# Optimization experiments

Measured on AMD Instinct MI355X. Metric: run time of the kernel, lower is better.

The kernel has to match this reference:

```python
import jax, jax.numpy as jnp
import numpy as np

K = 20          # knn neighbors (args.k)
BN_EPS = 1e-5   # torch BatchNorm default
LN_EPS = 1e-6


def _bn(x, g, b, axes):
    # training-mode batchnorm over `axes`, channel dim = 1
    m = x.mean(axes, keepdims=True)
    v = x.var(axes, keepdims=True)
    shp = [1] * x.ndim
    shp[1] = x.shape[1]
    return g.reshape(shp) * (x - m) * jax.lax.rsqrt(v + BN_EPS) + b.reshape(shp)


def _lrelu(x):
    return jnp.where(x >= 0, x, 0.2 * x)


def _graph_feature(x, k):
    # x: [B,C,N] -> [B,2C,N,k]  (knn gather + (neighbor-center, center) concat)
    B, C, N = x.shape
    inner = -2.0 * jnp.einsum('bcn,bcm->bnm', x, x)
    xx = jnp.sum(x * x, axis=1)                       # [B,N]
    pd = -xx[:, :, None] - inner - xx[:, None, :]     # negative sq. distance
    idx = jax.lax.top_k(pd, k)[1]                     # [B,N,k]
    xt = jnp.transpose(x, (0, 2, 1))                  # [B,N,C]
    feat = xt[jnp.arange(B)[:, None, None], idx]      # [B,N,k,C] gather
    ctr = xt[:, :, None, :]
    out = jnp.concatenate([feat - ctr, jnp.broadcast_to(ctr, feat.shape)], axis=-1)
    return jnp.transpose(out, (0, 3, 1, 2))


def _conv2d_block(x, w, g, b):
    # 1x1 conv2d (no bias) + BN2d + LeakyReLU(0.2)
    y = jnp.einsum('bcnk,oc->bonk', x, w)
    return _lrelu(_bn(y, g, b, (0, 2, 3)))


def _conv1d_block(x, w, g, b):
    y = jnp.einsum('bcl,oc->bol', x, w)
    return _lrelu(_bn(y, g, b, (0, 2)))


def _squash(t):
    sn = jnp.sum(t * t, axis=-1, keepdims=True)
    return sn * t / ((1.0 + sn) * jnp.sqrt(sn))


def _forward(data, l, dw1, dg1, db1, dw2, dg2, db2, dw3, dg3, db3,
             lin_w, ln_w, ln_b, caps_W,
             cw1, cg1, cb1, cw2, cg2, cb2, cw3, cw4, cg4, cb4, cw5, cg5, cb5):
    B, _, N = data.shape
    # ---- DGCNN encoder ----
    x = _conv2d_block(_graph_feature(data, K), dw1, dg1, db1)
    x1 = x.max(axis=-1)                               # [B,64,N]
    x = _conv2d_block(_graph_feature(x1, K), dw2, dg2, db2)
    x2 = x.max(axis=-1)                               # [B,64,N]
    x = _conv2d_block(_graph_feature(x2, K), dw3, dg3, db3)
    x3 = x.max(axis=-1)                               # [B,128,N]
    feat = jnp.transpose(jnp.concatenate([x1, x2, x3], axis=1), (0, 2, 1))  # [B,N,256]
    h = jnp.einsum('bnc,oc->bno', feat, lin_w)        # [B,N,40]
    mu = h.mean(axis=(1, 2), keepdims=True)
    var = h.var(axis=(1, 2), keepdims=True)
    encoder = jax.nn.relu(ln_w * (h - mu) * jax.lax.rsqrt(var + LN_EPS) + ln_b)  # [B,1024,40]
    # ---- Latent capsule layer (3-iter dynamic routing) ----
    u_hat = jnp.einsum('lpvd,bpd->blpv', caps_W, encoder)  # [B,40,1024,64]
    u_det = jax.lax.stop_gradient(u_hat)
    b_ij = jnp.zeros((B, caps_W.shape[0], caps_W.shape[1]), encoder.dtype)
    v = None
    for it in range(3):
        c = jax.nn.softmax(b_ij, axis=1)
        if it == 2:
            v = _squash(jnp.einsum('blp,blpv->blv', c, u_hat))
        else:
            v = _squash(jnp.einsum('blp,blpv->blv', c, u_det))
            b_ij = b_ij + jnp.einsum('blv,blpv->blp', v, u_det)
    latent = v                                        # [B,40,64]
    # ---- segmentation head ----
    emb = jnp.einsum('bpd,bdv->bpv', encoder, latent) # [B,1024,64]
    emb = emb.max(axis=-1, keepdims=True)             # [B,1024,1]
    lab = _conv1d_block(l.reshape(B, -1, 1), cw1, cg1, cb1)  # [B,64,1]
    emb = jnp.concatenate([emb, lab], axis=1)         # [B,1088,1]
    emb = jnp.tile(emb, (1, 1, N))                    # [B,1088,N]
    emb = jnp.concatenate([emb, jnp.transpose(encoder, (0, 2, 1))], axis=1)  # [B,1128,N]
    r = _conv1d_block(emb, cw2, cg2, cb2)
    r = _conv1d_block(r, cw3, cg2, cb2)               # conv3 shares bn2 params
    r = _conv1d_block(r, cw4, cg4, cb4)
    r = _conv1d_block(r, cw5, cg5, cb5)
    return r                                          # [B,50,N]


def setup_inputs() -> dict:
    key = jax.random.key(0)
    ks = jax.random.split(key, 16)
    B, N = 32, 1024
    f = jnp.float32
    rn = lambda k, s: 0.05 * jax.random.normal(k, s, dtype=f)
    return dict(
        data=jax.random.normal(ks[0], (B, 3, N), dtype=f),
        l=jax.random.uniform(ks[1], (B, 16), dtype=f),
        dw1=rn(ks[2], (64, 6)), dg1=jnp.ones(64, f), db1=jnp.zeros(64, f),
        dw2=rn(ks[3], (64, 128)), dg2=jnp.ones(64, f), db2=jnp.zeros(64, f),
        dw3=rn(ks[4], (128, 128)), dg3=jnp.ones(128, f), db3=jnp.zeros(128, f),
        lin_w=rn(ks[5], (40, 256)),
        ln_w=jnp.ones((N, 40), f), ln_b=jnp.zeros((N, 40), f),
        caps_W=0.01 * jax.random.normal(ks[6], (40, 1024, 64, 40), dtype=f),
        cw1=rn(ks[7], (64, 16)), cg1=jnp.ones(64, f), cb1=jnp.zeros(64, f),
        cw2=rn(ks[8], (256, 1128)), cg2=jnp.ones(256, f), cb2=jnp.zeros(256, f),
        cw3=rn(ks[9], (256, 256)),
        cw4=rn(ks[10], (128, 256)), cg4=jnp.ones(128, f), cb4=jnp.zeros(128, f),
        cw5=rn(ks[11], (50, 128)), cg5=jnp.ones(50, f), cb5=jnp.zeros(50, f),
    )


def reference(data, l, dw1, dg1, db1, dw2, dg2, db2, dw3, dg3, db3,
              lin_w, ln_w, ln_b, caps_W,
              cw1, cg1, cb1, cw2, cg2, cb2, cw3, cw4, cg4, cb4, cw5, cg5, cb5):
    return _forward(data, l, dw1, dg1, db1, dw2, dg2, db2, dw3, dg3, db3,
                    lin_w, ln_w, ln_b, caps_W,
                    cw1, cg1, cb1, cw2, cg2, cb2, cw3, cw4, cg4, cb4, cw5, cg5, cb5)
```

## Files before the change

### kernel.cpp

```cpp
#include <hip/hip_runtime.h>
#include <math.h>

constexpr int NB = 32, NN = 1024, KNN = 20;
constexpr int RTOT = NB * NN;

constexpr size_t SZ_BIG = (size_t)NB * NN * 40 * 64;
constexpr size_t O_BIG  = 0;
constexpr size_t O_XT0  = O_BIG + SZ_BIG;
constexpr size_t O_XT1  = O_XT0 + (size_t)RTOT * 4;
constexpr size_t O_XT2  = O_XT1 + (size_t)RTOT * 64;
constexpr size_t O_XT3  = O_XT2 + (size_t)RTOT * 64;
constexpr size_t O_XX   = O_XT3 + (size_t)RTOT * 128;
constexpr size_t O_IDX  = O_XX + RTOT;
constexpr size_t O_WC1  = O_IDX + (size_t)RTOT * KNN;
constexpr size_t O_WC2  = O_WC1 + 512;
constexpr size_t O_WC3  = O_WC2 + 8192;
constexpr size_t O_LWT  = O_WC3 + 16384;
constexpr size_t O_C2T  = O_LWT + 16384;
constexpr size_t O_C3T  = O_C2T + 10240;
constexpr size_t O_C4T  = O_C3T + 65536;
constexpr size_t O_C5T  = O_C4T + 32768;
constexpr size_t O_H    = O_C5T + 8192;
constexpr size_t O_LNST = O_H + (size_t)RTOT * 64;
constexpr size_t O_BSUM = O_LNST + 64;
constexpr size_t O_BSQ  = O_BSUM + 256;
constexpr size_t O_SCL  = O_BSQ + 256;
constexpr size_t O_SHF  = O_SCL + 256;
constexpr size_t O_SACC = O_SHF + 256;
constexpr size_t O_VB   = O_SACC + 81920;
constexpr size_t O_BIJ  = O_VB + 81920;
constexpr size_t O_EMB  = O_BIJ + (size_t)NB * 40 * NN;
constexpr size_t O_LAB  = O_EMB + RTOT;
constexpr size_t O_BASE = O_LAB + 2048;
constexpr size_t O_PS   = O_BIJ;
constexpr size_t O_PQ   = O_BIJ + 262144;
constexpr size_t O_PB   = O_XT1;
constexpr size_t O_PBU  = O_XT1;

__device__ __forceinline__ float lrelu(float z) { return fmaxf(z, 0.2f * z); }

__device__ __forceinline__ float key2f(unsigned u)
{
    unsigned b = (u & 0x80000000u) ? (u ^ 0x80000000u) : ~u;
    return __uint_as_float(b);
}

__global__ void k_wt(const float* __restrict__ src, float* __restrict__ dst,
                     int K, int On, int SS, int coff, int DS, int ooff, int Oreal)
{
    int i = blockIdx.x * 256 + threadIdx.x;
    if (i >= K * On) return;
    int c = i / On, o = i - c * On;
    dst[(size_t)c * DS + ooff + o] = (o < Oreal) ? src[(size_t)o * SS + coff + c] : 0.f;
}

__global__ void k_data_t(const float* __restrict__ d, float* __restrict__ xt)
{
    int i = blockIdx.x * 256 + threadIdx.x;
    if (i >= RTOT) return;
    int b = i >> 10, n = i & 1023;
#pragma unroll
    for (int c = 0; c < 3; ++c) xt[(size_t)i * 4 + c] = d[((size_t)b * 3 + c) * NN + n];
    xt[(size_t)i * 4 + 3] = 0.f;
}

template<int C, int CS>
__global__ void k_rownorm(const float* __restrict__ X, float* __restrict__ xx)
{
    int i = blockIdx.x * 256 + threadIdx.x;
    if (i >= RTOT) return;
    const float* p = X + (size_t)i * CS;
    float s = 0.f;
#pragma unroll
    for (int c = 0; c < C; ++c) s = fmaf(p[c], p[c], s);
    xx[i] = s;
}

template<int CS>
__global__ __launch_bounds__(256) void k_dist(const float* __restrict__ X,
    const float* __restrict__ xx, float* __restrict__ D)
{
    __shared__ float As[16][68];
    __shared__ float Bs[16][68];
    int b = blockIdx.z;
    int r0 = blockIdx.x * 64, m0 = blockIdx.y * 64;
    const float* Xb = X + (size_t)b * NN * CS;
    int t = threadIdx.x;
    int tx = t & 15, ty = t >> 4;
    float acc[4][4] = {};
    for (int k0 = 0; k0 < CS; k0 += 16) {
        __syncthreads();
        {
            int row = t >> 2, kb = (t & 3) * 4;
#pragma unroll
            for (int u = 0; u < 4; ++u) {
                int k = k0 + kb + u;
                As[kb + u][row] = (k < CS) ? Xb[(size_t)(r0 + row) * CS + k] : 0.f;
                Bs[kb + u][row] = (k < CS) ? Xb[(size_t)(m0 + row) * CS + k] : 0.f;
            }
        }
        __syncthreads();
#pragma unroll
        for (int k = 0; k < 16; ++k) {
            float4 a = *(const float4*)&As[k][ty * 4];
            float4 bb = *(const float4*)&Bs[k][tx * 4];
            float av[4] = {a.x, a.y, a.z, a.w};
            float bv[4] = {bb.x, bb.y, bb.z, bb.w};
#pragma unroll
            for (int i = 0; i < 4; ++i)
#pragma unroll
                for (int j = 0; j < 4; ++j)
                    acc[i][j] = fmaf(av[i], bv[j], acc[i][j]);
        }
    }
    const float* xxb = xx + b * NN + m0 + tx * 4;
    float x0 = xxb[0], x1 = xxb[1], x2 = xxb[2], x3 = xxb[3];
#pragma unroll
    for (int i = 0; i < 4; ++i) {
        float4 o4 = make_float4(2.f * acc[i][0] - x0, 2.f * acc[i][1] - x1,
                                2.f * acc[i][2] - x2, 2.f * acc[i][3] - x3);
        *(float4*)&D[((size_t)b * NN + r0 + ty * 4 + i) * NN + m0 + tx * 4] = o4;
    }
}

__global__ __launch_bounds__(256) void k_sel(const float* __restrict__ D,
                                             int* __restrict__ idxb)
{
    int gw = blockIdx.x * 4 + (threadIdx.x >> 6);
    int lane = threadIdx.x & 63;
    const float* drow = D + (size_t)gw * NN;
    float vr[16];
#pragma unroll
    for (int j = 0; j < 16; ++j) vr[j] = drow[j * 64 + lane];

    unsigned lo = 0x007FFFFFu;
    unsigned hi = 0xFF800000u;
#pragma unroll 1
    while (hi - lo > 1u) {
        unsigned mid = lo + ((hi - lo) >> 1);
        float tm = key2f(mid);
        int c = 0;
#pragma unroll
        for (int j = 0; j < 16; ++j) c += __popcll(__ballot(vr[j] > tm));
        if (c < KNN) hi = mid; else lo = mid;
    }
    float t = key2f(hi);

    int* outp = idxb + (size_t)gw * KNN;
    unsigned long long mylow = (1ull << lane) - 1ull;
    int base = 0;
#pragma unroll
    for (int j = 0; j < 16; ++j) {
        unsigned long long bmask = __ballot(vr[j] > t);
        if (vr[j] > t) outp[base + __popcll(bmask & mylow)] = j * 64 + lane;
        base += __popcll(bmask);
    }
#pragma unroll 1
    for (int j = 0; j < 16 && base < KNN; ++j) {
        unsigned long long bmask = __ballot(vr[j] == t);
        int pre = __popcll(bmask & mylow);
        if (vr[j] == t && base + pre < KNN) outp[base + pre] = j * 64 + lane;
        base += __popcll(bmask);
    }
}

template<bool ACT, bool BIAS>
__global__ __launch_bounds__(256) void k_gemm(const float* __restrict__ X,
    const float* __restrict__ W, float* __restrict__ Y, int K, int OC, int XS,
    const float* __restrict__ scale, const float* __restrict__ shift,
    const float* __restrict__ bias)
{
    __shared__ float Xs[16][68];
    __shared__ float Ws[16][64];
    int r0 = blockIdx.x * 64, o0 = blockIdx.y * 64;
    int t = threadIdx.x;
    int tx = t & 15, ty = t >> 4;
    float acc[4][4] = {};
    for (int k0 = 0; k0 < K; k0 += 16) {
        __syncthreads();
        {
            int row = t >> 2, kb = (t & 3) * 4;
#pragma unroll
            for (int u = 0; u < 4; ++u) {
                int k = k0 + kb + u;
                float v = 0.f;
                if (k < K) {
                    v = X[(size_t)(r0 + row) * XS + k];
                    if (ACT) { float z = fmaf(v, scale[k], shift[k]); v = fmaxf(z, 0.2f * z); }
                }
                Xs[kb + u][row] = v;
            }
            int kw = t >> 4, ow = (t & 15) * 4;
            float4 wv = make_float4(0.f, 0.f, 0.f, 0.f);
            if (k0 + kw < K) wv = *(const float4*)&W[(size_t)(k0 + kw) * OC + o0 + ow];
            *(float4*)&Ws[kw][ow] = wv;
        }
        __syncthreads();
#pragma unroll
        for (int k = 0; k < 16; ++k) {
            float4 a = *(const float4*)&Xs[k][ty * 4];
            float4 bb = *(const float4*)&Ws[k][tx * 4];
            float av[4] = {a.x, a.y, a.z, a.w};
            float bvv[4] = {bb.x, bb.y, bb.z, bb.w};
#pragma unroll
            for (int i = 0; i < 4; ++i)
#pragma unroll
                for (int j = 0; j < 4; ++j)
                    acc[i][j] = fmaf(av[i], bvv[j], acc[i][j]);
        }
    }
#pragma unroll
    for (int i = 0; i < 4; ++i) {
        int r = r0 + ty * 4 + i;
        float4 o4;
        float* po = (float*)&o4;
#pragma unroll
        for (int j = 0; j < 4; ++j) {
            float v = acc[i][j];
            if (BIAS) v += bias[(size_t)(r >> 10) * OC + o0 + tx * 4 + j];
            po[j] = v;
        }
        *(float4*)&Y[(size_t)r * OC + o0 + tx * 4] = o4;
    }
}

template<int O>
__global__ __launch_bounds__(256) void k_gather(const float* __restrict__ Z,
    const int* __restrict__ idxb, float* __restrict__ xo,
    float* __restrict__ part_s, float* __restrict__ part_q)
{
    constexpr int OL = O / 64;
    __shared__ float rs[4][O], rq[4][O];
    int b = blockIdx.y, nt = blockIdx.x;
    int t = threadIdx.x, lane = t & 63, w = t >> 6;
    float ps[OL] = {}, pq[OL] = {};
    for (int i = 0; i < 4; ++i) {
        int n = nt * 16 + w * 4 + i;
        size_t r = (size_t)b * NN + n;
        float zd[OL], ym[OL];
#pragma unroll
        for (int j = 0; j < OL; ++j) {
            int o = lane + j * 64;
            zd[j] = Z[r * (2 * O) + O + o] - Z[r * (2 * O) + o];
            ym[j] = -3.4e38f;
        }
        int midx[KNN];
        {
            const int4* ip = (const int4*)&idxb[r * KNN];
#pragma unroll
            for (int q = 0; q < 5; ++q) {
                int4 t4 = ip[q];
                midx[4 * q + 0] = t4.x; midx[4 * q + 1] = t4.y;
                midx[4 * q + 2] = t4.z; midx[4 * q + 3] = t4.w;
            }
        }
#pragma unroll
        for (int k = 0; k < KNN; ++k) {
            size_t rm = (size_t)b * NN + midx[k];
#pragma unroll
            for (int j = 0; j < OL; ++j) {
                float y = Z[rm * (2 * O) + lane + j * 64] + zd[j];
                ym[j] = fmaxf(ym[j], y);
                ps[j] += y; pq[j] = fmaf(y, y, pq[j]);
            }
        }
#pragma unroll
        for (int j = 0; j < OL; ++j) xo[r * O + lane + j * 64] = ym[j];
    }
#pragma unroll
    for (int j = 0; j < OL; ++j) { rs[w][lane + j * 64] = ps[j]; rq[w][lane + j * 64] = pq[j]; }
    __syncthreads();
    if (w == 0) {
        int blk = blockIdx.y * 64 + blockIdx.x;
#pragma unroll
        for (int j = 0; j < OL; ++j) {
            int o = lane + j * 64;
            part_s[(size_t)o * 2048 + blk] = rs[0][o] + rs[1][o] + rs[2][o] + rs[3][o];
            part_q[(size_t)o * 2048 + blk] = rq[0][o] + rq[1][o] + rq[2][o] + rq[3][o];
        }
    }
}

__global__ void k_bnfin2(const float* __restrict__ part_s, const float* __restrict__ part_q,
                         const float* __restrict__ g, const float* __restrict__ bb,
                         float* __restrict__ scale, float* __restrict__ shift,
                         int OC, float invM, float eps)
{
    int o = blockIdx.x * blockDim.x + threadIdx.x;
    if (o >= OC) return;
    const float* ps = part_s + (size_t)o * 2048;
    const float* pq = part_q + (size_t)o * 2048;
    float s0 = 0.f, s1 = 0.f, s2 = 0.f, s3 = 0.f;
    float q0 = 0.f, q1 = 0.f, q2 = 0.f, q3 = 0.f;
    for (int i = 0; i < 2048; i += 4) {
        s0 += ps[i]; s1 += ps[i + 1]; s2 += ps[i + 2]; s3 += ps[i + 3];
        q0 += pq[i]; q1 += pq[i + 1]; q2 += pq[i + 2]; q3 += pq[i + 3];
    }
    float s = (s0 + s1) + (s2 + s3);
    float q = (q0 + q1) + (q2 + q3);
    float mu = s * invM;
    float var = q * invM - mu * mu;
    float sc = g[o] * rsqrtf(var + eps);
    scale[o] = sc; shift[o] = bb[o] - mu * sc;
}

__global__ void k_bnfin(const float* __restrict__ sums, const float* __restrict__ sumsq,
                        const float* __restrict__ g, const float* __restrict__ bb,
                        float* __restrict__ scale, float* __restrict__ shift,
                        int OC, float invM, float eps)
{
    int o = blockIdx.x * blockDim.x + threadIdx.x;
    if (o >= OC) return;
    float mu = sums[o] * invM;
    float var = sumsq[o] * invM - mu * mu;
    float sc = g[o] * rsqrtf(var + eps);
    scale[o] = sc; shift[o] = bb[o] - mu * sc;
}

__global__ void k_bnapply(float* __restrict__ x, const float* __restrict__ scale,
                          const float* __restrict__ shift, int total, int O)
{
    int i = blockIdx.x * 256 + threadIdx.x;
    if (i >= total) return;
    int o = i & (O - 1);
    x[i] = lrelu(fmaf(x[i], scale[o], shift[o]));
}

__global__ void k_concat(const float* __restrict__ x1, const float* __restrict__ x2,
                         const float* __restrict__ x3, float* __restrict__ f)
{
    int i = blockIdx.x * 256 + threadIdx.x;
    if (i >= RTOT * 256) return;
    int r = i >> 8, c = i & 255;
    float v;
    if (c < 64) v = x1[(size_t)r * 64 + c];
    else if (c < 128) v = x2[(size_t)r * 64 + c - 64];
    else v = x3[(size_t)r * 128 + c - 128];
    f[(size_t)i] = v;
}

__global__ __launch_bounds__(256) void k_lnstats(const float* __restrict__ h, float* __restrict__ st)
{
    __shared__ float rsm[256], rqm[256];
    int b = blockIdx.x, t = threadIdx.x;
    float s = 0.f, q = 0.f;
    for (int i = t; i < 40960; i += 256) {
        int n = i / 40, o = i - n * 40;
        float v = h[((size_t)b * NN + n) * 64 + o];
        s += v; q = fmaf(v, v, q);
    }
    rsm[t] = s; rqm[t] = q; __syncthreads();
    for (int off = 128; off; off >>= 1) {
        if (t < off) { rsm[t] += rsm[t + off]; rqm[t] += rqm[t + off]; }
        __syncthreads();
    }
    if (t == 0) {
        float mu = rsm[0] / 40960.f;
        float var = rqm[0] / 40960.f - mu * mu;
        st[2 * b] = mu; st[2 * b + 1] = rsqrtf(var + 1e-6f);
    }
}

__global__ void k_lnapply(float* __restrict__ h, const float* __restrict__ lnw,
                          const float* __restrict__ lnb, const float* __restrict__ st)
{
    int i = blockIdx.x * 256 + threadIdx.x;
    if (i >= NB * NN * 40) return;
    int b = i / 40960, rem = i - b * 40960, n = rem / 40, o = rem - n * 40;
    float mu = st[2 * b], rstd = st[2 * b + 1];
    size_t a = ((size_t)b * NN + n) * 64 + o;
    float v = fmaf((h[a] - mu) * rstd, lnw[n * 40 + o], lnb[n * 40 + o]);
    h[a] = fmaxf(v, 0.f);
}

__global__ __launch_bounds__(64) void k_uhat(const float* __restrict__ enc,
    const float* __restrict__ caps, float* __restrict__ U, float* __restrict__ pbu)
{
    __shared__ float clt[40 * 68];
    int pc = blockIdx.x, l = blockIdx.y;
    int lane = threadIdx.x;
    int vg = lane & 7, bg = lane >> 3;
    int v0 = vg * 8, b0 = bg * 4;
    float spart[4][8] = {};
#pragma unroll 1
    for (int pi = 0; pi < 16; ++pi) {
        int p = pc * 16 + pi;
        const float4* cp4 = (const float4*)(caps + ((size_t)l * NN + p) * 2560);
#pragma unroll
        for (int k = 0; k < 10; ++k) {
            int i4 = lane + k * 64;
            float4 cv = cp4[i4];
            int e0 = i4 * 4;
            int v = e0 / 40;
            int d0 = e0 - v * 40;
            clt[(d0 + 0) * 68 + v] = cv.x;
            clt[(d0 + 1) * 68 + v] = cv.y;
            clt[(d0 + 2) * 68 + v] = cv.z;
            clt[(d0 + 3) * 68 + v] = cv.w;
        }
        float acc[4][8] = {};
#pragma unroll
        for (int d4 = 0; d4 < 10; ++d4) {
            float4 e4[4];
#pragma unroll
            for (int i = 0; i < 4; ++i)
                e4[i] = *(const float4*)&enc[((size_t)(b0 + i) * NN + p) * 64 + d4 * 4];
#pragma unroll
            for (int dd = 0; dd < 4; ++dd) {
                int d = d4 * 4 + dd;
                float4 c0 = *(const float4*)&clt[d * 68 + v0];
                float4 c1 = *(const float4*)&clt[d * 68 + v0 + 4];
                float cv[8] = {c0.x, c0.y, c0.z, c0.w, c1.x, c1.y, c1.z, c1.w};
#pragma unroll
                for (int i = 0; i < 4; ++i) {
                    float e = ((const float*)&e4[i])[dd];
#pragma unroll
                    for (int j = 0; j < 8; ++j)
                        acc[i][j] = fmaf(e, cv[j], acc[i][j]);
                }
            }
        }
#pragma unroll
        for (int i = 0; i < 4; ++i) {
            float* up = &U[((size_t)(b0 + i) * NN + p) * 2560 + l * 64 + v0];
            float4 o0 = make_float4(acc[i][0], acc[i][1], acc[i][2], acc[i][3]);
            float4 o1 = make_float4(acc[i][4], acc[i][5], acc[i][6], acc[i][7]);
            *(float4*)up = o0;
            *(float4*)(up + 4) = o1;
#pragma unroll
            for (int j = 0; j < 8; ++j) spart[i][j] += acc[i][j];
        }
    }
    float* pb = pbu + (size_t)pc * 81920;
#pragma unroll
    for (int i = 0; i < 4; ++i) {
        float4 s0 = make_float4(spart[i][0], spart[i][1], spart[i][2], spart[i][3]);
        float4 s1 = make_float4(spart[i][4], spart[i][5], spart[i][6], spart[i][7]);
        float* dst = &pb[(size_t)(b0 + i) * 2560 + l * 64 + v0];
        *(float4*)dst = s0;
        *(float4*)(dst + 4) = s1;
    }
}

template<int MODE>
__global__ __launch_bounds__(256, 4) void k_route(const float* __restrict__ U,
    const float* __restrict__ vprev, const float* __restrict__ bin,
    float* __restrict__ bout, float* __restrict__ pbuf)
{
    __shared__ float vl[2560];
    __shared__ float red[4][1280];
    int b = blockIdx.x, pc = blockIdx.y;
    int t = threadIdx.x, lane = t & 63, w = t >> 6;
    for (int i = t; i < 2560; i += 256) vl[i] = vprev[(size_t)b * 2560 + i];
    __syncthreads();
    float4 acc[10];
#pragma unroll
    for (int it = 0; it < 10; ++it) acc[it] = make_float4(0.f, 0.f, 0.f, 0.f);
    int lgrp = lane >> 4;
#pragma unroll 1
    for (int pi = 0; pi < 8; ++pi) {
        int p = pc * 32 + w * 8 + pi;
        const float4* up4 = (const float4*)(U + ((size_t)b * NN + p) * 2560);
        float4 u[10];
#pragma unroll
        for (int it = 0; it < 10; ++it) u[it] = up4[it * 64 + lane];
        float pd[10];
#pragma unroll
        for (int it = 0; it < 10; ++it) {
            float4 vv = *(const float4*)&vl[it * 256 + lane * 4];
            float s = u[it].x * vv.x;
            s = fmaf(u[it].y, vv.y, s);
            s = fmaf(u[it].z, vv.z, s);
            s = fmaf(u[it].w, vv.w, s);
            s += __shfl_xor(s, 1, 64);
            s += __shfl_xor(s, 2, 64);
            s += __shfl_xor(s, 4, 64);
            s += __shfl_xor(s, 8, 64);
            pd[it] = s;
        }
        if (MODE == 1) {
            if ((lane & 15) == 0) {
#pragma unroll
                for (int it = 0; it < 10; ++it)
                    bout[((size_t)b * 40 + it * 4 + lgrp) * NN + p] = pd[it];
            }
        } else {
#pragma unroll
            for (int it = 0; it < 10; ++it)
                pd[it] += bin[((size_t)b * 40 + it * 4 + lgrp) * NN + p];
        }
        float mx = -3.4e38f;
#pragma unroll
        for (int it = 0; it < 10; ++it) {
            float m = pd[it];
            m = fmaxf(m, __shfl_xor(m, 16, 64));
            m = fmaxf(m, __shfl_xor(m, 32, 64));
            mx = fmaxf(mx, m);
        }
        float eo[10]; float se = 0.f;
#pragma unroll
        for (int it = 0; it < 10; ++it) {
            float e = expf(pd[it] - mx);
            eo[it] = e;
            float sg = e;
            sg += __shfl_xor(sg, 16, 64);
            sg += __shfl_xor(sg, 32, 64);
            se += sg;
        }
        float inv = 1.f / se;
#pragma unroll
        for (int it = 0; it < 10; ++it) {
            float wgt = eo[it] * inv;
            acc[it].x = fmaf(wgt, u[it].x, acc[it].x);
            acc[it].y = fmaf(wgt, u[it].y, acc[it].y);
            acc[it].z = fmaf(wgt, u[it].z, acc[it].z);
            acc[it].w = fmaf(wgt, u[it].w, acc[it].w);
        }
    }
    float* pb = pbuf + ((size_t)pc * NB + b) * 2560;
#pragma unroll 1
    for (int h = 0; h < 2; ++h) {
        __syncthreads();
#pragma unroll
        for (int it = 0; it < 5; ++it)
            *(float4*)&red[w][it * 256 + lane * 4] = acc[h * 5 + it];
        __syncthreads();
        if (w == 0) {
#pragma unroll
            for (int it = 0; it < 5; ++it) {
                int idx = it * 256 + lane * 4;
                float4 a0 = *(const float4*)&red[0][idx];
                float4 a1 = *(const float4*)&red[1][idx];
                float4 a2 = *(const float4*)&red[2][idx];
                float4 a3 = *(const float4*)&red[3][idx];
                float4 o = make_float4((a0.x + a1.x) + (a2.x + a3.x),
                                       (a0.y + a1.y) + (a2.y + a3.y),
                                       (a0.z + a1.z) + (a2.z + a3.z),
                                       (a0.w + a1.w) + (a2.w + a3.w));
                *(float4*)&pb[h * 1280 + idx] = o;
            }
        }
    }
}

template<int NCH>
__global__ void k_sredN(const float* __restrict__ pbuf, float* __restrict__ sac)
{
    int i4 = blockIdx.x * 256 + threadIdx.x;
    if (i4 >= NB * 640) return;
    const float4* pb4 = (const float4*)pbuf;
    float4 s = make_float4(0.f, 0.f, 0.f, 0.f);
#pragma unroll 4
    for (int pc = 0; pc < NCH; ++pc) {
        float4 v = pb4[(size_t)pc * (NB * 640) + i4];
        s.x += v.x; s.y += v.y; s.z += v.z; s.w += v.w;
    }
    ((float4*)sac)[i4] = s;
}

__global__ void k_squash(const float* __restrict__ s_in, float* __restrict__ vout, float premul)
{
    int i = blockIdx.x * 256 + threadIdx.x;
    if (i >= NB * 40) return;
    const float* sp = s_in + (size_t)i * 64;
    float* vp = vout + (size_t)i * 64;
    float sn = 0.f;
    for (int v = 0; v < 64; ++v) { float tv = sp[v] * premul; sn = fmaf(tv, tv, sn); }
    float f = sn / ((1.f + sn) * sqrtf(sn));
    for (int v = 0; v < 64; ++v) vp[v] = sp[v] * premul * f;
}

__global__ __launch_bounds__(256) void k_emb(const float* __restrict__ enc,
    const float* __restrict__ lat, float* __restrict__ embm)
{
    __shared__ float latl[2560];
    int b = blockIdx.x, pt = blockIdx.y;
    int t = threadIdx.x, lane = t & 63, w = t >> 6;
    for (int i = t; i < 2560; i += 256) latl[i] = lat[(size_t)b * 2560 + i];
    __syncthreads();
    for (int i = 0; i < 32; ++i) {
        int p = pt * 128 + w * 32 + i;
        const float* ep = enc + ((size_t)b * NN + p) * 64;
        float acc = 0.f;
#pragma unroll
        for (int d = 0; d < 40; ++d) acc = fmaf(ep[d], latl[d * 64 + lane], acc);
        float mx = acc;
#pragma unroll
        for (int s = 32; s; s >>= 1) mx = fmaxf(mx, __shfl_xor(mx, s, 64));
        if (lane == 0) embm[(size_t)b * NN + p] = mx;
    }
}

__global__ __launch_bounds__(64) void k_lab(const float* __restrict__ lin,
    const float* __restrict__ w, const float* __restrict__ g, const float* __restrict__ bb,
    float* __restrict__ lab)
{
    int o = threadIdx.x;
    float ys[32]; float s = 0.f, q = 0.f;
#pragma unroll
    for (int b = 0; b < 32; ++b) {
        float y = 0.f;
#pragma unroll
        for (int c = 0; c < 16; ++c) y = fmaf(lin[b * 16 + c], w[o * 16 + c], y);
        ys[b] = y; s += y; q = fmaf(y, y, q);
    }
    float mu = s / 32.f, var = q / 32.f - mu * mu;
    float sc = g[o] * rsqrtf(var + 1e-5f);
    float sh = bb[o] - mu * sc;
#pragma unroll
    for (int b = 0; b < 32; ++b) lab[b * 64 + o] = lrelu(fmaf(ys[b], sc, sh));
}

__global__ __launch_bounds__(256) void k_base2(const float* __restrict__ em,
    const float* __restrict__ lab, const float* __restrict__ cw2, float* __restrict__ base)
{
    __shared__ float eml[1024];
    __shared__ float lbl[64];
    int b = blockIdx.x, t = threadIdx.x;
    for (int i = t; i < 1024; i += 256) eml[i] = em[(size_t)b * NN + i];
    if (t < 64) lbl[t] = lab[b * 64 + t];
    __syncthreads();
    const float* wr = cw2 + (size_t)t * 1128;
    float acc = 0.f;
    for (int c = 0; c < 1024; ++c) acc = fmaf(wr[c], eml[c], acc);
#pragma unroll
    for (int c = 0; c < 64; ++c) acc = fmaf(wr[1024 + c], lbl[c], acc);
    base[b * 256 + t] = acc;
}

__global__ __launch_bounds__(256) void k_colstats(const float* __restrict__ Y,
    float* __restrict__ sums, float* __restrict__ sumsq, int OC)
{
    __shared__ float rs[4][64], rq[4][64];
    int chunk = blockIdx.x, o0 = blockIdx.y * 64;
    int t = threadIdx.x, lane = t & 63, w = t >> 6;
    int o = o0 + lane;
    float s = 0.f, q = 0.f;
    for (int j = 0; j < 64; ++j) {
        int r = chunk * 256 + w * 64 + j;
        float v = Y[(size_t)r * OC + o];
        s += v; q = fmaf(v, v, q);
    }
    rs[w][lane] = s; rq[w][lane] = q;
    __syncthreads();
    if (w == 0) {
        atomicAdd(&sums[o], rs[0][lane] + rs[1][lane] + rs[2][lane] + rs[3][lane]);
        atomicAdd(&sumsq[o], rq[0][lane] + rq[1][lane] + rq[2][lane] + rq[3][lane]);
    }
}

__global__ void k_out(const float* __restrict__ Y, const float* __restrict__ scale,
                      const float* __restrict__ shift, float* __restrict__ out)
{
    int i = blockIdx.x * 256 + threadIdx.x;
    if (i >= NB * 50 * NN) return;
    int n = i & 1023, rest = i >> 10;
    int o = rest % 50, b = rest / 50;
    float y = Y[((size_t)b * NN + n) * 64 + o];
    out[i] = lrelu(fmaf(y, scale[o], shift[o]));
}

extern "C" void kernel_launch(void* const* d_in, const int* in_sizes, int n_in,
                              void* d_out, int out_size, void* d_ws, size_t ws_size,
                              hipStream_t stream)
{
    const float* data = (const float*)d_in[0];
    const float* lin  = (const float*)d_in[1];
    const float* dw1  = (const float*)d_in[2];
    const float* dg1  = (const float*)d_in[3];
    const float* db1  = (const float*)d_in[4];
    const float* dw2  = (const float*)d_in[5];
    const float* dg2  = (const float*)d_in[6];
    const float* db2  = (const float*)d_in[7];
    const float* dw3  = (const float*)d_in[8];
    const float* dg3  = (const float*)d_in[9];
    const float* db3  = (const float*)d_in[10];
    const float* lw   = (const float*)d_in[11];
    const float* lnw  = (const float*)d_in[12];
    const float* lnb  = (const float*)d_in[13];
    const float* caps = (const float*)d_in[14];
    const float* cw1  = (const float*)d_in[15];
    const float* cg1  = (const float*)d_in[16];
    const float* cb1  = (const float*)d_in[17];
    const float* cw2  = (const float*)d_in[18];
    const float* cg2  = (const float*)d_in[19];
    const float* cb2  = (const float*)d_in[20];
    const float* cw3  = (const float*)d_in[21];
    const float* cw4  = (const float*)d_in[22];
    const float* cg4  = (const float*)d_in[23];
    const float* cb4  = (const float*)d_in[24];
    const float* cw5  = (const float*)d_in[25];
    const float* cg5  = (const float*)d_in[26];
    const float* cb5  = (const float*)d_in[27];
    float* out = (float*)d_out;
    float* ws = (float*)d_ws;

    float* big  = ws + O_BIG;
    float* xt0  = ws + O_XT0;
    float* xt1  = ws + O_XT1;
    float* xt2  = ws + O_XT2;
    float* xt3  = ws + O_XT3;
    float* xxp  = ws + O_XX;
    int*   idxb = (int*)(ws + O_IDX);
    float* wc1  = ws + O_WC1;
    float* wc2  = ws + O_WC2;
    float* wc3  = ws + O_WC3;
    float* lwt  = ws + O_LWT;
    float* c2t  = ws + O_C2T;
    float* c3t  = ws + O_C3T;
    float* c4t  = ws + O_C4T;
    float* c5t  = ws + O_C5T;
    float* hbuf = ws + O_H;
    float* lnst = ws + O_LNST;
    float* bsum = ws + O_BSUM;
    float* bsq  = ws + O_BSQ;
    float* scl  = ws + O_SCL;
    float* shf  = ws + O_SHF;
    float* sac  = ws + O_SACC;
    float* vb   = ws + O_VB;
    float* bij  = ws + O_BIJ;
    float* embm = ws + O_EMB;
    float* labp = ws + O_LAB;
    float* basep= ws + O_BASE;
    float* psP  = ws + O_PS;
    float* pqP  = ws + O_PQ;
    float* pbuf = ws + O_PB;
    float* pbu  = ws + O_PBU;
    float* Dbuf = big;
    float* Z    = big;
    float* U    = big;
    float* yb1  = big;
    float* yb2  = big + 8388608;

    k_wt<<<1,   256, 0, stream>>>(dw1, wc1, 3, 64, 6, 0, 128, 0, 64);
    k_wt<<<1,   256, 0, stream>>>(dw1, wc1, 3, 64, 6, 3, 128, 64, 64);
    k_wt<<<16,  256, 0, stream>>>(dw2, wc2, 64, 64, 128, 0, 128, 0, 64);
    k_wt<<<16,  256, 0, stream>>>(dw2, wc2, 64, 64, 128, 64, 128, 64, 64);
    k_wt<<<32,  256, 0, stream>>>(dw3, wc3, 64, 128, 128, 0, 256, 0, 128);
    k_wt<<<32,  256, 0, stream>>>(dw3, wc3, 64, 128, 128, 64, 256, 128, 128);
    k_wt<<<64,  256, 0, stream>>>(lw,  lwt, 256, 64, 256, 0, 64, 0, 40);
    k_wt<<<40,  256, 0, stream>>>(cw2, c2t, 40, 256, 1128, 1088, 256, 0, 256);
    k_wt<<<256, 256, 0, stream>>>(cw3, c3t, 256, 256, 256, 0, 256, 0, 256);
    k_wt<<<128, 256, 0, stream>>>(cw4, c4t, 256, 128, 256, 0, 128, 0, 128);
    k_wt<<<32,  256, 0, stream>>>(cw5, c5t, 128, 64, 128, 0, 64, 0, 50);
    k_data_t<<<128, 256, 0, stream>>>(data, xt0);

    k_rownorm<3, 4><<<128, 256, 0, stream>>>(xt0, xxp);
    k_dist<4><<<dim3(16, 16, 32), 256, 0, stream>>>(xt0, xxp, Dbuf);
    k_sel<<<8192, 256, 0, stream>>>(Dbuf, idxb);
    k_gemm<false, false><<<dim3(512, 2), 256, 0, stream>>>(xt0, wc1, Z, 3, 128, 4, nullptr, nullptr, nullptr);
    k_gather<64><<<dim3(64, 32), 256, 0, stream>>>(Z, idxb, xt1, psP, pqP);
    k_bnfin2<<<1, 64, 0, stream>>>(psP, pqP, dg1, db1, scl, shf, 64, 1.f / 655360.f, 1e-5f);
    k_bnapply<<<8192, 256, 0, stream>>>(xt1, scl, shf, RTOT * 64, 64);

    k_rownorm<64, 64><<<128, 256, 0, stream>>>(xt1, xxp);
    k_dist<64><<<dim3(16, 16, 32), 256, 0, stream>>>(xt1, xxp, Dbuf);
    k_sel<<<8192, 256, 0, stream>>>(Dbuf, idxb);
    k_gemm<false, false><<<dim3(512, 2), 256, 0, stream>>>(xt1, wc2, Z, 64, 128, 64, nullptr, nullptr, nullptr);
    k_gather<64><<<dim3(64, 32), 256, 0, stream>>>(Z, idxb, xt2, psP, pqP);
    k_bnfin2<<<1, 64, 0, stream>>>(psP, pqP, dg2, db2, scl, shf, 64, 1.f / 655360.f, 1e-5f);
    k_bnapply<<<8192, 256, 0, stream>>>(xt2, scl, shf, RTOT * 64, 64);

    k_rownorm<64, 64><<<128, 256, 0, stream>>>(xt2, xxp);
    k_dist<64><<<dim3(16, 16, 32), 256, 0, stream>>>(xt2, xxp, Dbuf);
    k_sel<<<8192, 256, 0, stream>>>(Dbuf, idxb);
    k_gemm<false, false><<<dim3(512, 4), 256, 0, stream>>>(xt2, wc3, Z, 64, 256, 64, nullptr, nullptr, nullptr);
    k_gather<128><<<dim3(64, 32), 256, 0, stream>>>(Z, idxb, xt3, psP, pqP);
    k_bnfin2<<<1, 128, 0, stream>>>(psP, pqP, dg3, db3, scl, shf, 128, 1.f / 655360.f, 1e-5f);
    k_bnapply<<<16384, 256, 0, stream>>>(xt3, scl, shf, RTOT * 128, 128);

    k_concat<<<32768, 256, 0, stream>>>(xt1, xt2, xt3, big);
    k_gemm<false, false><<<dim3(512, 1), 256, 0, stream>>>(big, lwt, hbuf, 256, 64, 256, nullptr, nullptr, nullptr);
    k_lnstats<<<32, 256, 0, stream>>>(hbuf, lnst);
    k_lnapply<<<5120, 256, 0, stream>>>(hbuf, lnw, lnb, lnst);

    k_uhat<<<dim3(64, 40), 64, 0, stream>>>(hbuf, caps, U, pbu);
    k_sredN<64><<<80, 256, 0, stream>>>(pbu, sac);
    k_squash<<<5, 256, 0, stream>>>(sac, vb, 1.f / 40.f);
    k_route<1><<<dim3(32, 32), 256, 0, stream>>>(U, vb, nullptr, bij, pbuf);
    k_sredN<32><<<80, 256, 0, stream>>>(pbuf, sac);
    k_squash<<<5, 256, 0, stream>>>(sac, vb, 1.f);
    k_route<2><<<dim3(32, 32), 256, 0, stream>>>(U, vb, bij, nullptr, pbuf);
    k_sredN<32><<<80, 256, 0, stream>>>(pbuf, sac);
    k_squash<<<5, 256, 0, stream>>>(sac, vb, 1.f);

    k_emb<<<dim3(32, 8), 256, 0, stream>>>(hbuf, vb, embm);
    k_lab<<<1, 64, 0, stream>>>(lin, cw1, cg1, cb1, labp);
    k_base2<<<32, 256, 0, stream>>>(embm, labp, cw2, basep);

    k_gemm<false, true><<<dim3(512, 4), 256, 0, stream>>>(hbuf, c2t, yb1, 40, 256, 64, nullptr, nullptr, basep);
    hipMemsetAsync(bsum, 0, 512 * 4, stream);
    k_colstats<<<dim3(128, 4), 256, 0, stream>>>(yb1, bsum, bsq, 256);
    k_bnfin<<<1, 256, 0, stream>>>(bsum, bsq, cg2, cb2, scl, shf, 256, 1.f / 32768.f, 1e-5f);

    k_gemm<true, false><<<dim3(512, 4), 256, 0, stream>>>(yb1, c3t, yb2, 256, 256, 256, scl, shf, nullptr);
    hipMemsetAsync(bsum, 0, 512 * 4, stream);
    k_colstats<<<dim3(128, 4), 256, 0, stream>>>(yb2, bsum, bsq, 256);
    k_bnfin<<<1, 256, 0, stream>>>(bsum, bsq, cg2, cb2, scl, shf, 256, 1.f / 32768.f, 1e-5f);

    k_gemm<true, false><<<dim3(512, 2), 256, 0, stream>>>(yb2, c4t, yb1, 256, 128, 256, scl, shf, nullptr);
    hipMemsetAsync(bsum, 0, 512 * 4, stream);
    k_colstats<<<dim3(128, 2), 256, 0, stream>>>(yb1, bsum, bsq, 128);
    k_bnfin<<<1, 256, 0, stream>>>(bsum, bsq, cg4, cb4, scl, shf, 128, 1.f / 32768.f, 1e-5f);

    k_gemm<true, false><<<dim3(512, 1), 256, 0, stream>>>(yb1, c5t, yb2, 128, 64, 128, scl, shf, nullptr);
    hipMemsetAsync(bsum, 0, 512 * 4, stream);
    k_colstats<<<dim3(128, 1), 256, 0, stream>>>(yb2, bsum, bsq, 64);
    k_bnfin<<<1, 256, 0, stream>>>(bsum, bsq, cg5, cb5, scl, shf, 50, 1.f / 32768.f, 1e-5f);

    k_out<<<6400, 256, 0, stream>>>(yb2, scl, shf, out);
}
```

Measured before the change: 1.755 ms.

## Fuse small kernels to cut launch count and drop atomics/memsets in BN stats

Merges the eleven weight-transpose launches into one kernel and folds the row-norm computation into the data transpose and BN-apply kernels. Squash is fused into the capsule partial-sum reduction, and the label MLP is merged into k_base2. Column statistics now write per-chunk partials that bnfin3 reduces, which removes the atomics and memsets. The aim is to cut launch overhead and extra passes over memory, at the cost of k_base2 recomputing the label BN in every block.

Result: faster. 1.708 ms (-2.6%).

```diff
diff --git a/kernel.cpp b/kernel.cpp
--- a/kernel.cpp
+++ b/kernel.cpp
@@ -45,34 +45,50 @@
     return __uint_as_float(b);
 }
 
-__global__ void k_wt(const float* __restrict__ src, float* __restrict__ dst,
-                     int K, int On, int SS, int coff, int DS, int ooff, int Oreal)
-{
-    int i = blockIdx.x * 256 + threadIdx.x;
+__device__ __forceinline__ void wt_do(const float* __restrict__ src, float* __restrict__ dst,
+                                      int i, int K, int On, int SS, int coff, int DS, int ooff, int Oreal)
+{
     if (i >= K * On) return;
     int c = i / On, o = i - c * On;
     dst[(size_t)c * DS + ooff + o] = (o < Oreal) ? src[(size_t)o * SS + coff + c] : 0.f;
 }
 
-__global__ void k_data_t(const float* __restrict__ d, float* __restrict__ xt)
+__global__ __launch_bounds__(256) void k_wtall(
+    const float* __restrict__ dw1, const float* __restrict__ dw2, const float* __restrict__ dw3,
+    const float* __restrict__ lw,  const float* __restrict__ cw2, const float* __restrict__ cw3,
+    const float* __restrict__ cw4, const float* __restrict__ cw5,
+    float* __restrict__ wc1, float* __restrict__ wc2, float* __restrict__ wc3,
+    float* __restrict__ lwt, float* __restrict__ c2t, float* __restrict__ c3t,
+    float* __restrict__ c4t, float* __restrict__ c5t)
+{
+    int bid = blockIdx.x, t = threadIdx.x;
+    if      (bid < 1)   wt_do(dw1, wc1, (bid - 0) * 256 + t,   3, 64, 6, 0, 128, 0, 64);
+    else if (bid < 2)   wt_do(dw1, wc1, (bid - 1) * 256 + t,   3, 64, 6, 3, 128, 64, 64);
+    else if (bid < 18)  wt_do(dw2, wc2, (bid - 2) * 256 + t,   64, 64, 128, 0, 128, 0, 64);
+    else if (bid < 34)  wt_do(dw2, wc2, (bid - 18) * 256 + t,  64, 64, 128, 64, 128, 64, 64);
+    else if (bid < 66)  wt_do(dw3, wc3, (bid - 34) * 256 + t,  64, 128, 128, 0, 256, 0, 128);
+    else if (bid < 98)  wt_do(dw3, wc3, (bid - 66) * 256 + t,  64, 128, 128, 64, 256, 128, 128);
+    else if (bid < 162) wt_do(lw,  lwt, (bid - 98) * 256 + t,  256, 64, 256, 0, 64, 0, 40);
+    else if (bid < 202) wt_do(cw2, c2t, (bid - 162) * 256 + t, 40, 256, 1128, 1088, 256, 0, 256);
+    else if (bid < 458) wt_do(cw3, c3t, (bid - 202) * 256 + t, 256, 256, 256, 0, 256, 0, 256);
+    else if (bid < 586) wt_do(cw4, c4t, (bid - 458) * 256 + t, 256, 128, 256, 0, 128, 0, 128);
+    else                wt_do(cw5, c5t, (bid - 586) * 256 + t, 128, 64, 128, 0, 64, 0, 50);
+}
+
+__global__ void k_data_t(const float* __restrict__ d, float* __restrict__ xt,
+                         float* __restrict__ xx)
 {
     int i = blockIdx.x * 256 + threadIdx.x;
     if (i >= RTOT) return;
     int b = i >> 10, n = i & 1023;
-#pragma unroll
-    for (int c = 0; c < 3; ++c) xt[(size_t)i * 4 + c] = d[((size_t)b * 3 + c) * NN + n];
+    float s = 0.f;
+#pragma unroll
+    for (int c = 0; c < 3; ++c) {
+        float v = d[((size_t)b * 3 + c) * NN + n];
+        xt[(size_t)i * 4 + c] = v;
+        s = fmaf(v, v, s);
+    }
     xt[(size_t)i * 4 + 3] = 0.f;
-}
-
-template<int C, int CS>
-__global__ void k_rownorm(const float* __restrict__ X, float* __restrict__ xx)
-{
-    int i = blockIdx.x * 256 + threadIdx.x;
-    if (i >= RTOT) return;
-    const float* p = X + (size_t)i * CS;
-    float s = 0.f;
-#pragma unroll
-    for (int c = 0; c < C; ++c) s = fmaf(p[c], p[c], s);
     xx[i] = s;
 }
 
@@ -304,15 +320,25 @@
     scale[o] = sc; shift[o] = bb[o] - mu * sc;
 }
 
-__global__ void k_bnfin(const float* __restrict__ sums, const float* __restrict__ sumsq,
-                        const float* __restrict__ g, const float* __restrict__ bb,
-                        float* __restrict__ scale, float* __restrict__ shift,
-                        int OC, float invM, float eps)
+__global__ void k_bnfin3(const float* __restrict__ part_s, const float* __restrict__ part_q,
+                         const float* __restrict__ g, const float* __restrict__ bb,
+                         float* __restrict__ scale, float* __restrict__ shift,
+                         int OC, float invM, float eps)
 {
     int o = blockIdx.x * blockDim.x + threadIdx.x;
     if (o >= OC) return;
-    float mu = sums[o] * invM;
-    float var = sumsq[o] * invM - mu * mu;
+    const float* ps = part_s + (size_t)o * 128;
+    const float* pq = part_q + (size_t)o * 128;
+    float s0 = 0.f, s1 = 0.f, s2 = 0.f, s3 = 0.f;
+    float q0 = 0.f, q1 = 0.f, q2 = 0.f, q3 = 0.f;
+    for (int i = 0; i < 128; i += 4) {
+        s0 += ps[i]; s1 += ps[i + 1]; s2 += ps[i + 2]; s3 += ps[i + 3];
+        q0 += pq[i]; q1 += pq[i + 1]; q2 += pq[i + 2]; q3 += pq[i + 3];
+    }
+    float s = (s0 + s1) + (s2 + s3);
+    float q = (q0 + q1) + (q2 + q3);
+    float mu = s * invM;
+    float var = q * invM - mu * mu;
     float sc = g[o] * rsqrtf(var + eps);
     scale[o] = sc; shift[o] = bb[o] - mu * sc;
 }
@@ -324,6 +350,32 @@
     if (i >= total) return;
     int o = i & (O - 1);
     x[i] = lrelu(fmaf(x[i], scale[o], shift[o]));
+}
+
+__global__ __launch_bounds__(256) void k_bnapply_rn(float* __restrict__ x,
+    const float* __restrict__ scale, const float* __restrict__ shift,
+    float* __restrict__ xx)
+{
+    __shared__ float red[16][17];
+    int t = threadIdx.x;
+    int i4 = blockIdx.x * 256 + t;
+    int q = t & 15, lrow = t >> 4;
+    float4 v = ((float4*)x)[i4];
+    int o = q * 4;
+    v.x = lrelu(fmaf(v.x, scale[o + 0], shift[o + 0]));
+    v.y = lrelu(fmaf(v.y, scale[o + 1], shift[o + 1]));
+    v.z = lrelu(fmaf(v.z, scale[o + 2], shift[o + 2]));
+    v.w = lrelu(fmaf(v.w, scale[o + 3], shift[o + 3]));
+    ((float4*)x)[i4] = v;
+    float part = fmaf(v.w, v.w, fmaf(v.z, v.z, fmaf(v.y, v.y, v.x * v.x)));
+    red[lrow][q] = part;
+    __syncthreads();
+    if (t < 16) {
+        float s = 0.f;
+#pragma unroll
+        for (int j = 0; j < 16; ++j) s += red[t][j];
+        xx[blockIdx.x * 16 + t] = s;
+    }
 }
 
 __global__ void k_concat(const float* __restrict__ x1, const float* __restrict__ x2,
@@ -544,10 +596,14 @@
 }
 
 template<int NCH>
-__global__ void k_sredN(const float* __restrict__ pbuf, float* __restrict__ sac)
-{
-    int i4 = blockIdx.x * 256 + threadIdx.x;
-    if (i4 >= NB * 640) return;
+__global__ __launch_bounds__(256) void k_sredsq(const float* __restrict__ pbuf,
+    float* __restrict__ vout, float premul)
+{
+    __shared__ float red[16][17];
+    __shared__ float fac[16];
+    int t = threadIdx.x;
+    int i4 = blockIdx.x * 256 + t;
+    int q = t & 15, lrow = t >> 4;
     const float4* pb4 = (const float4*)pbuf;
     float4 s = make_float4(0.f, 0.f, 0.f, 0.f);
 #pragma unroll 4
@@ -555,19 +611,19 @@
         float4 v = pb4[(size_t)pc * (NB * 640) + i4];
         s.x += v.x; s.y += v.y; s.z += v.z; s.w += v.w;
     }
-    ((float4*)sac)[i4] = s;
-}
-
-__global__ void k_squash(const float* __restrict__ s_in, float* __restrict__ vout, float premul)
-{
-    int i = blockIdx.x * 256 + threadIdx.x;
-    if (i >= NB * 40) return;
-    const float* sp = s_in + (size_t)i * 64;
-    float* vp = vout + (size_t)i * 64;
-    float sn = 0.f;
-    for (int v = 0; v < 64; ++v) { float tv = sp[v] * premul; sn = fmaf(tv, tv, sn); }
-    float f = sn / ((1.f + sn) * sqrtf(sn));
-    for (int v = 0; v < 64; ++v) vp[v] = sp[v] * premul * f;
+    s.x *= premul; s.y *= premul; s.z *= premul; s.w *= premul;
+    float part = fmaf(s.w, s.w, fmaf(s.z, s.z, fmaf(s.y, s.y, s.x * s.x)));
+    red[lrow][q] = part;
+    __syncthreads();
+    if (t < 16) {
+        float sn = 0.f;
+#pragma unroll
+        for (int j = 0; j < 16; ++j) sn += red[t][j];
+        fac[t] = sn / ((1.f + sn) * sqrtf(sn));
+    }
+    __syncthreads();
+    float f = fac[lrow];
+    ((float4*)vout)[i4] = make_float4(s.x * f, s.y * f, s.z * f, s.w * f);
 }
 
 __global__ __launch_bounds__(256) void k_emb(const float* __restrict__ enc,
@@ -591,34 +647,30 @@
     }
 }
 
-__global__ __launch_bounds__(64) void k_lab(const float* __restrict__ lin,
-    const float* __restrict__ w, const float* __restrict__ g, const float* __restrict__ bb,
-    float* __restrict__ lab)
-{
-    int o = threadIdx.x;
-    float ys[32]; float s = 0.f, q = 0.f;
-#pragma unroll
-    for (int b = 0; b < 32; ++b) {
-        float y = 0.f;
-#pragma unroll
-        for (int c = 0; c < 16; ++c) y = fmaf(lin[b * 16 + c], w[o * 16 + c], y);
-        ys[b] = y; s += y; q = fmaf(y, y, q);
-    }
-    float mu = s / 32.f, var = q / 32.f - mu * mu;
-    float sc = g[o] * rsqrtf(var + 1e-5f);
-    float sh = bb[o] - mu * sc;
-#pragma unroll
-    for (int b = 0; b < 32; ++b) lab[b * 64 + o] = lrelu(fmaf(ys[b], sc, sh));
-}
-
 __global__ __launch_bounds__(256) void k_base2(const float* __restrict__ em,
-    const float* __restrict__ lab, const float* __restrict__ cw2, float* __restrict__ base)
+    const float* __restrict__ lin, const float* __restrict__ cw1,
+    const float* __restrict__ cg1, const float* __restrict__ cb1,
+    const float* __restrict__ cw2, float* __restrict__ base)
 {
     __shared__ float eml[1024];
     __shared__ float lbl[64];
     int b = blockIdx.x, t = threadIdx.x;
     for (int i = t; i < 1024; i += 256) eml[i] = em[(size_t)b * NN + i];
-    if (t < 64) lbl[t] = lab[b * 64 + t];
+    if (t < 64) {
+        int o = t;
+        float ys[32]; float s = 0.f, q = 0.f;
+#pragma unroll
+        for (int bb = 0; bb < 32; ++bb) {
+            float y = 0.f;
+#pragma unroll
+            for (int c = 0; c < 16; ++c) y = fmaf(lin[bb * 16 + c], cw1[o * 16 + c], y);
+            ys[bb] = y; s += y; q = fmaf(y, y, q);
+        }
+        float mu = s / 32.f, var = q / 32.f - mu * mu;
+        float sc = cg1[o] * rsqrtf(var + 1e-5f);
+        float sh = cb1[o] - mu * sc;
+        lbl[o] = lrelu(fmaf(ys[b], sc, sh));
+    }
     __syncthreads();
     const float* wr = cw2 + (size_t)t * 1128;
     float acc = 0.f;
@@ -628,8 +680,8 @@
     base[b * 256 + t] = acc;
 }
 
-__global__ __launch_bounds__(256) void k_colstats(const float* __restrict__ Y,
-    float* __restrict__ sums, float* __restrict__ sumsq, int OC)
+__global__ __launch_bounds__(256) void k_colstats2(const float* __restrict__ Y,
+    float* __restrict__ part_s, float* __restrict__ part_q, int OC)
 {
     __shared__ float rs[4][64], rq[4][64];
     int chunk = blockIdx.x, o0 = blockIdx.y * 64;
@@ -644,8 +696,8 @@
     rs[w][lane] = s; rq[w][lane] = q;
     __syncthreads();
     if (w == 0) {
-        atomicAdd(&sums[o], rs[0][lane] + rs[1][lane] + rs[2][lane] + rs[3][lane]);
-        atomicAdd(&sumsq[o], rq[0][lane] + rq[1][lane] + rq[2][lane] + rq[3][lane]);
+        part_s[(size_t)o * 128 + chunk] = rs[0][lane] + rs[1][lane] + rs[2][lane] + rs[3][lane];
+        part_q[(size_t)o * 128 + chunk] = rq[0][lane] + rq[1][lane] + rq[2][lane] + rq[3][lane];
     }
 }
 
@@ -712,15 +764,11 @@
     float* c5t  = ws + O_C5T;
     float* hbuf = ws + O_H;
     float* lnst = ws + O_LNST;
-    float* bsum = ws + O_BSUM;
-    float* bsq  = ws + O_BSQ;
     float* scl  = ws + O_SCL;
     float* shf  = ws + O_SHF;
-    float* sac  = ws + O_SACC;
     float* vb   = ws + O_VB;
     float* bij  = ws + O_BIJ;
     float* embm = ws + O_EMB;
-    float* labp = ws + O_LAB;
     float* basep= ws + O_BASE;
     float* psP  = ws + O_PS;
     float* pqP  = ws + O_PQ;
@@ -732,36 +780,24 @@
     float* yb1  = big;
     float* yb2  = big + 8388608;
 
-    k_wt<<<1,   256, 0, stream>>>(dw1, wc1, 3, 64, 6, 0, 128, 0, 64);
-    k_wt<<<1,   256, 0, stream>>>(dw1, wc1, 3, 64, 6, 3, 128, 64, 64);
-    k_wt<<<16,  256, 0, stream>>>(dw2, wc2, 64, 64, 128, 0, 128, 0, 64);
-    k_wt<<<16,  256, 0, stream>>>(dw2, wc2, 64, 64, 128, 64, 128, 64, 64);
-    k_wt<<<32,  256, 0, stream>>>(dw3, wc3, 64, 128, 128, 0, 256, 0, 128);
-    k_wt<<<32,  256, 0, stream>>>(dw3, wc3, 64, 128, 128, 64, 256, 128, 128);
-    k_wt<<<64,  256, 0, stream>>>(lw,  lwt, 256, 64, 256, 0, 64, 0, 40);
-    k_wt<<<40,  256, 0, stream>>>(cw2, c2t, 40, 256, 1128, 1088, 256, 0, 256);
-    k_wt<<<256, 256, 0, stream>>>(cw3, c3t, 256, 256, 256, 0, 256, 0, 256);
-    k_wt<<<128, 256, 0, stream>>>(cw4, c4t, 256, 128, 256, 0, 128, 0, 128);
-    k_wt<<<32,  256, 0, stream>>>(cw5, c5t, 128, 64, 128, 0, 64, 0, 50);
-    k_data_t<<<128, 256, 0, stream>>>(data, xt0);
-
-    k_rownorm<3, 4><<<128, 256, 0, stream>>>(xt0, xxp);
+    k_wtall<<<618, 256, 0, stream>>>(dw1, dw2, dw3, lw, cw2, cw3, cw4, cw5,
+                                     wc1, wc2, wc3, lwt, c2t, c3t, c4t, c5t);
+    k_data_t<<<128, 256, 0, stream>>>(data, xt0, xxp);
+
     k_dist<4><<<dim3(16, 16, 32), 256, 0, stream>>>(xt0, xxp, Dbuf);
     k_sel<<<8192, 256, 0, stream>>>(Dbuf, idxb);
     k_gemm<false, false><<<dim3(512, 2), 256, 0, stream>>>(xt0, wc1, Z, 3, 128, 4, nullptr, nullptr, nullptr);
     k_gather<64><<<dim3(64, 32), 256, 0, stream>>>(Z, idxb, xt1, psP, pqP);
     k_bnfin2<<<1, 64, 0, stream>>>(psP, pqP, dg1, db1, scl, shf, 64, 1.f / 655360.f, 1e-5f);
-    k_bnapply<<<8192, 256, 0, stream>>>(xt1, scl, shf, RTOT * 64, 64);
-
-    k_rownorm<64, 64><<<128, 256, 0, stream>>>(xt1, xxp);
+    k_bnapply_rn<<<2048, 256, 0, stream>>>(xt1, scl, shf, xxp);
+
     k_dist<64><<<dim3(16, 16, 32), 256, 0, stream>>>(xt1, xxp, Dbuf);
     k_sel<<<8192, 256, 0, stream>>>(Dbuf, idxb);
     k_gemm<false, false><<<dim3(512, 2), 256, 0, stream>>>(xt1, wc2, Z, 64, 128, 64, nullptr, nullptr, nullptr);
     k_gather<64><<<dim3(64, 32), 256, 0, stream>>>(Z, idxb, xt2, psP, pqP);
     k_bnfin2<<<1, 64, 0, stream>>>(psP, pqP, dg2, db2, scl, shf, 64, 1.f / 655360.f, 1e-5f);
-    k_bnapply<<<8192, 256, 0, stream>>>(xt2, scl, shf, RTOT * 64, 64);
-
-    k_rownorm<64, 64><<<128, 256, 0, stream>>>(xt2, xxp);
+    k_bnapply_rn<<<2048, 256, 0, stream>>>(xt2, scl, shf, xxp);
+
     k_dist<64><<<dim3(16, 16, 32), 256, 0, stream>>>(xt2, xxp, Dbuf);
     k_sel<<<8192, 256, 0, stream>>>(Dbuf, idxb);
     k_gemm<false, false><<<dim3(512, 4), 256, 0, stream>>>(xt2, wc3, Z, 64, 256, 64, nullptr, nullptr, nullptr);
@@ -775,38 +811,30 @@
     k_lnapply<<<5120, 256, 0, stream>>>(hbuf, lnw, lnb, lnst);
 
     k_uhat<<<dim3(64, 40), 64, 0, stream>>>(hbuf, caps, U, pbu);
-    k_sredN<64><<<80, 256, 0, stream>>>(pbu, sac);
-    k_squash<<<5, 256, 0, stream>>>(sac, vb, 1.f / 40.f);
+    k_sredsq<64><<<80, 256, 0, stream>>>(pbu, vb, 1.f / 40.f);
     k_route<1><<<dim3(32, 32), 256, 0, stream>>>(U, vb, nullptr, bij, pbuf);
-    k_sredN<32><<<80, 256, 0, stream>>>(pbuf, sac);
-    k_squash<<<5, 256, 0, stream>>>(sac, vb, 1.f);
+    k_sredsq<32><<<80, 256, 0, stream>>>(pbuf, vb, 1.f);
     k_route<2><<<dim3(32, 32), 256, 0, stream>>>(U, vb, bij, nullptr, pbuf);
-    k_sredN<32><<<80, 256, 0, stream>>>(pbuf, sac);
-    k_squash<<<5, 256, 0, stream>>>(sac, vb, 1.f);
+    k_sredsq<32><<<80, 256, 0, stream>>>(pbuf, vb, 1.f);
 
     k_emb<<<dim3(32, 8), 256, 0, stream>>>(hbuf, vb, embm);
-    k_lab<<<1, 64, 0, stream>>>(lin, cw1, cg1, cb1, labp);
-    k_base2<<<32, 256, 0, stream>>>(embm, labp, cw2, basep);
+    k_base2<<<32, 256, 0, stream>>>(embm, lin, cw1, cg1, cb1, cw2, basep);
 
     k_gemm<false, true><<<dim3(512, 4), 256, 0, stream>>>(hbuf, c2t, yb1, 40, 256, 64, nullptr, nullptr, basep);
-    hipMemsetAsync(bsum, 0, 512 * 4, stream);
-    k_colstats<<<dim3(128, 4), 256, 0, stream>>>(yb1, bsum, bsq, 256);
-    k_bnfin<<<1, 256, 0, stream>>>(bsum, bsq, cg2, cb2, scl, shf, 256, 1.f / 32768.f, 1e-5f);
+    k_colstats2<<<dim3(128, 4), 256, 0, stream>>>(yb1, psP, pqP, 256);
+    k_bnfin3<<<1, 256, 0, stream>>>(psP, pqP, cg2, cb2, scl, shf, 256, 1.f / 32768.f, 1e-5f);
 
     k_gemm<true, false><<<dim3(512, 4), 256, 0, stream>>>(yb1, c3t, yb2, 256, 256, 256, scl, shf, nullptr);
-    hipMemsetAsync(bsum, 0, 512 * 4, stream);
-    k_colstats<<<dim3(128, 4), 256, 0, stream>>>(yb2, bsum, bsq, 256);
-    k_bnfin<<<1, 256, 0, stream>>>(bsum, bsq, cg2, cb2, scl, shf, 256, 1.f / 32768.f, 1e-5f);
+    k_colstats2<<<dim3(128, 4), 256, 0, stream>>>(yb2, psP, pqP, 256);
+    k_bnfin3<<<1, 256, 0, stream>>>(psP, pqP, cg2, cb2, scl, shf, 256, 1.f / 32768.f, 1e-5f);
 
     k_gemm<true, false><<<dim3(512, 2), 256, 0, stream>>>(yb2, c4t, yb1, 256, 128, 256, scl, shf, nullptr);
-    hipMemsetAsync(bsum, 0, 512 * 4, stream);
-    k_colstats<<<dim3(128, 2), 256, 0, stream>>>(yb1, bsum, bsq, 128);
-    k_bnfin<<<1, 256, 0, stream>>>(bsum, bsq, cg4, cb4, scl, shf, 128, 1.f / 32768.f, 1e-5f);
+    k_colstats2<<<dim3(128, 2), 256, 0, stream>>>(yb1, psP, pqP, 128);
+    k_bnfin3<<<1, 256, 0, stream>>>(psP, pqP, cg4, cb4, scl, shf, 128, 1.f / 32768.f, 1e-5f);
 
     k_gemm<true, false><<<dim3(512, 1), 256, 0, stream>>>(yb1, c5t, yb2, 128, 64, 128, scl, shf, nullptr);
-    hipMemsetAsync(bsum, 0, 512 * 4, stream);
-    k_colstats<<<dim3(128, 1), 256, 0, stream>>>(yb2, bsum, bsq, 64);
-    k_bnfin<<<1, 256, 0, stream>>>(bsum, bsq, cg5, cb5, scl, shf, 50, 1.f / 32768.f, 1e-5f);
+    k_colstats2<<<dim3(128, 1), 256, 0, stream>>>(yb2, psP, pqP, 64);
+    k_bnfin3<<<1, 256, 0, stream>>>(psP, pqP, cg5, cb5, scl, shf, 50, 1.f / 32768.f, 1e-5f);
 
     k_out<<<6400, 256, 0, stream>>>(yb2, scl, shf, out);
 }
```
